# Optimization experiments

Measured on AMD Instinct MI355X. Metric: run time of the kernel, lower is better.

The kernel has to match this reference:

```python
import jax, jax.numpy as jnp
import numpy as np

N = 32768      # number of nodes (joint candidates)
DIN = 128      # NODE_INPUT_DIM
H1 = 128       # OUTPUT_SIZES[0]
DOUT = 128     # OUTPUT_SIZES[-1] == output_dim
T = 17         # number of node types / expert MLPs


def setup_inputs() -> dict:
    key = jax.random.key(0)
    ks = jax.random.split(key, 6)
    x = jax.random.normal(ks[0], (N, DIN), dtype=jnp.float32)
    node_types = jax.random.randint(ks[1], (N,), 0, T)
    # Stacked per-type MLP parameters (17 independent Linear-ReLU-Linear MLPs).
    W1 = jax.random.normal(ks[2], (T, DIN, H1), dtype=jnp.float32) / np.float32(np.sqrt(DIN))
    b1 = jax.random.normal(ks[3], (T, H1), dtype=jnp.float32) * 0.01
    W2 = jax.random.normal(ks[4], (T, H1, DOUT), dtype=jnp.float32) / np.float32(np.sqrt(H1))
    b2 = jax.random.normal(ks[5], (T, DOUT), dtype=jnp.float32) * 0.01
    return {"x": x, "W1": W1, "b1": b1, "W2": W2, "b2": b2, "node_types": node_types}


def reference(x, W1, b1, W2, b2, node_types):
    # Dense hard-routing: evaluate all 17 type-specific MLPs on every node,
    # then select each node's own type. Mathematically identical to the
    # boolean-mask gather/scatter loop in the torch module (each row of the
    # output is MLP_{node_types[n]}(x[n])), but fully vectorized and jittable.
    h = jax.nn.relu(jnp.einsum('nd,tdh->nth', x, W1) + b1)   # [N, T, H1]
    y = jnp.einsum('nth,thm->ntm', h, W2) + b2               # [N, T, DOUT]
    # gather the row matching each node's type (combine step)
    out = jnp.take_along_axis(y, node_types[:, None, None], axis=1)[:, 0, :]  # [N, DOUT]
    return out
```

## Files before the change

### kernel.cpp

```cpp
#include <hip/hip_runtime.h>

#define N_NODES 32768
#define NB 128
#define DIM 128
#define NT 17
#define ROWS 64
#define BPT 48
#define LP 136

typedef short bf16x8 __attribute__((ext_vector_type(8)));
typedef float f32x4 __attribute__((ext_vector_type(4)));

#define WS_BLOCKHIST 0
#define WS_TL        8704
#define WS_W1T       74240
#define WS_W2T       631296

__device__ __forceinline__ unsigned short f2bf(float f) {
  unsigned int u = __float_as_uint(f);
  u += 0x7FFFu + ((u >> 16) & 1u);
  return (unsigned short)(u >> 16);
}

__global__ void k_pre(const int* __restrict__ types, int* __restrict__ blockHist,
                      unsigned short* __restrict__ tl,
                      const float* __restrict__ W1, const float* __restrict__ W2,
                      unsigned short* __restrict__ W1t, unsigned short* __restrict__ W2t) {
  int tid = threadIdx.x;
  if (blockIdx.x < NB) {
    __shared__ int h[NT];
    if (tid < NT) h[tid] = 0;
    __syncthreads();
    int i = blockIdx.x * 256 + tid;
    int ty = types[i];
    int r = atomicAdd(&h[ty], 1);
    tl[i] = (unsigned short)(ty | (r << 5));
    __syncthreads();
    if (tid < NT) blockHist[blockIdx.x * NT + tid] = h[tid];
    return;
  }
  int m = blockIdx.x - NB;
  const float* src = (m < NT) ? (W1 + (size_t)m * DIM * DIM)
                              : (W2 + (size_t)(m - NT) * DIM * DIM);
  unsigned short* dst = (m < NT) ? (W1t + (size_t)m * DIM * DIM)
                                 : (W2t + (size_t)(m - NT) * DIM * DIM);
  __shared__ unsigned short tile[DIM * LP];
  #pragma unroll
  for (int it = 0; it < 32; ++it) {
    int s = tid + it * 256;
    int n = s & 127, kp = s >> 7;
    float a = src[(size_t)(2 * kp) * DIM + n];
    float b = src[(size_t)(2 * kp + 1) * DIM + n];
    unsigned int pk = (unsigned int)f2bf(a) | ((unsigned int)f2bf(b) << 16);
    *(unsigned int*)&tile[n * LP + 2 * kp] = pk;
  }
  __syncthreads();
  #pragma unroll
  for (int it = 0; it < 8; ++it) {
    int s = tid + it * 256;
    int n = s >> 4, c = s & 15;
    *(uint4*)(dst + (size_t)n * DIM + c * 8) = *(const uint4*)&tile[n * LP + c * 8];
  }
}

__global__ __launch_bounds__(256, 3)
void k_mlp(const float* __restrict__ x, const float* __restrict__ b1,
           const float* __restrict__ b2, float* __restrict__ out,
           const int* __restrict__ blockHist, const unsigned short* __restrict__ tl,
           const unsigned short* __restrict__ W1t, const unsigned short* __restrict__ W2t) {
  int t = blockIdx.y;
  int tid = threadIdx.x;

  __shared__ int cc[NB];
  __shared__ int prow[ROWS];
  __shared__ unsigned short Xs[ROWS * LP];
  __shared__ unsigned short Ws[DIM * LP];

  int v = 0;
  if (tid < NB) { v = blockHist[tid * NT + t]; cc[tid] = v; }
  #pragma unroll
  for (int off = 1; off < NB; off <<= 1) {
    __syncthreads();
    int add = (tid < NB && tid >= off) ? cc[tid - off] : 0;
    __syncthreads();
    if (tid < NB) { v += add; cc[tid] = v; }
  }
  __syncthreads();
  int total = cc[NB - 1];
  int win_lo = blockIdx.x * ROWS;
  if (win_lo >= total) return;
  int win_hi = win_lo + ROWS;
  int nvalid = min(ROWS, total - win_lo);

  if (tid < ROWS) prow[tid] = 0;
  __syncthreads();

  int lo = 0, hi = NB;
  while (lo < hi) { int mid = (lo + hi) >> 1; if (cc[mid] > win_lo) hi = mid; else lo = mid + 1; }
  for (int b = lo; b < NB; ++b) {
    int excl = b ? cc[b - 1] : 0;
    if (excl >= win_hi) break;
    unsigned short pv = tl[b * 256 + tid];
    int ty = pv & 31, lr = pv >> 5;
    int g = excl + lr;
    if (ty == t && g >= win_lo && g < win_hi) prow[g - win_lo] = b * 256 + tid;
  }
  __syncthreads();

  #pragma unroll
  for (int it = 0; it < 8; ++it) {
    int s = tid + it * 256;
    int r = s >> 5, c4 = s & 31;
    int rr = (r < nvalid) ? r : 0;
    const float4 vx = *(const float4*)(x + (size_t)prow[rr] * DIM + c4 * 4);
    unsigned int lo2 = (unsigned int)f2bf(vx.x) | ((unsigned int)f2bf(vx.y) << 16);
    unsigned int hi2 = (unsigned int)f2bf(vx.z) | ((unsigned int)f2bf(vx.w) << 16);
    *(uint2*)&Xs[r * LP + c4 * 4] = make_uint2(lo2, hi2);
  }
  const unsigned short* w1g = W1t + (size_t)t * DIM * DIM;
  #pragma unroll
  for (int it = 0; it < 8; ++it) {
    int s = tid + it * 256;
    int n = s >> 4, c = s & 15;
    *(uint4*)&Ws[n * LP + c * 8] = *(const uint4*)(w1g + n * DIM + c * 8);
  }
  __syncthreads();

  int lane = tid & 63, w = tid >> 6;
  int l15 = lane & 15, q = lane >> 4;
  int arow = w * 16 + l15;
  int kb = q * 8;

  f32x4 acc[8];
  #pragma unroll
  for (int nt = 0; nt < 8; ++nt) acc[nt] = (f32x4){0.f, 0.f, 0.f, 0.f};
  #pragma unroll
  for (int kk = 0; kk < 4; ++kk) {
    bf16x8 a = *(const bf16x8*)&Xs[arow * LP + kk * 32 + kb];
    #pragma unroll
    for (int nt = 0; nt < 8; ++nt) {
      bf16x8 b = *(const bf16x8*)&Ws[(nt * 16 + l15) * LP + kk * 32 + kb];
      acc[nt] = __builtin_amdgcn_mfma_f32_16x16x32_bf16(a, b, acc[nt], 0, 0, 0);
    }
  }
  const float* b1t = b1 + t * DIM;
  #pragma unroll
  for (int nt = 0; nt < 8; ++nt) {
    int col = nt * 16 + l15;
    float bias = b1t[col];
    #pragma unroll
    for (int r = 0; r < 4; ++r) {
      int row = w * 16 + q * 4 + r;
      Xs[row * LP + col] = f2bf(fmaxf(acc[nt][r] + bias, 0.f));
    }
  }
  __syncthreads();

  const unsigned short* w2g = W2t + (size_t)t * DIM * DIM;
  #pragma unroll
  for (int it = 0; it < 8; ++it) {
    int s = tid + it * 256;
    int n = s >> 4, c = s & 15;
    *(uint4*)&Ws[n * LP + c * 8] = *(const uint4*)(w2g + n * DIM + c * 8);
  }
  __syncthreads();

  #pragma unroll
  for (int nt = 0; nt < 8; ++nt) acc[nt] = (f32x4){0.f, 0.f, 0.f, 0.f};
  #pragma unroll
  for (int kk = 0; kk < 4; ++kk) {
    bf16x8 a = *(const bf16x8*)&Xs[arow * LP + kk * 32 + kb];
    #pragma unroll
    for (int nt = 0; nt < 8; ++nt) {
      bf16x8 b = *(const bf16x8*)&Ws[(nt * 16 + l15) * LP + kk * 32 + kb];
      acc[nt] = __builtin_amdgcn_mfma_f32_16x16x32_bf16(a, b, acc[nt], 0, 0, 0);
    }
  }
  const float* b2t = b2 + t * DIM;
  int r0 = w * 16 + q * 4;
  int gr[4]; bool vld[4];
  #pragma unroll
  for (int r = 0; r < 4; ++r) {
    vld[r] = (r0 + r) < nvalid;
    gr[r] = prow[r0 + r];
  }
  #pragma unroll
  for (int nt = 0; nt < 8; ++nt) {
    int col = nt * 16 + l15;
    float bias = b2t[col];
    #pragma unroll
    for (int r = 0; r < 4; ++r) {
      if (vld[r]) out[(size_t)gr[r] * DIM + col] = acc[nt][r] + bias;
    }
  }
}

extern "C" void kernel_launch(void* const* d_in, const int* in_sizes, int n_in,
                              void* d_out, int out_size, void* d_ws, size_t ws_size,
                              hipStream_t stream) {
  const float* x  = (const float*)d_in[0];
  const float* W1 = (const float*)d_in[1];
  const float* b1 = (const float*)d_in[2];
  const float* W2 = (const float*)d_in[3];
  const float* b2 = (const float*)d_in[4];
  const int* types = (const int*)d_in[5];
  float* out = (float*)d_out;

  char* ws = (char*)d_ws;
  int* blockHist = (int*)(ws + WS_BLOCKHIST);
  unsigned short* tl  = (unsigned short*)(ws + WS_TL);
  unsigned short* W1t = (unsigned short*)(ws + WS_W1T);
  unsigned short* W2t = (unsigned short*)(ws + WS_W2T);

  k_pre<<<NB + 2 * NT, 256, 0, stream>>>(types, blockHist, tl, W1, W2, W1t, W2t);
  dim3 grid(BPT, NT);
  k_mlp<<<grid, 256, 0, stream>>>(x, b1, b2, out, blockHist, tl, W1t, W2t);
}
```

Baseline: 94.65 us.

## Double rows per block to 128 and prefetch type-list loads in gather loop

Each block now handles 128 rows of a node type instead of 64, with each wave computing two 16-row MFMA tiles that share each loaded weight fragment. This halves the number of blocks that each reload the per-type W1/W2 tiles into LDS and the per-block scan/search overhead. The row-gather loop now software-prefetches the next type-list chunk, and the zeroing of the prow array before it is removed. Occupancy hint drops from 3 to 2 blocks per CU, and the larger tile means fewer blocks and more padding waste on partially filled windows.

```diff
diff --git a/kernel.cpp b/kernel.cpp
--- a/kernel.cpp
+++ b/kernel.cpp
@@ -4,8 +4,8 @@
 #define NB 128
 #define DIM 128
 #define NT 17
-#define ROWS 64
-#define BPT 48
+#define ROWS 128
+#define BPT 24
 #define LP 136
 
 typedef short bf16x8 __attribute__((ext_vector_type(8)));
@@ -63,7 +63,7 @@
   }
 }
 
-__global__ __launch_bounds__(256, 3)
+__global__ __launch_bounds__(256, 2)
 void k_mlp(const float* __restrict__ x, const float* __restrict__ b1,
            const float* __restrict__ b2, float* __restrict__ out,
            const int* __restrict__ blockHist, const unsigned short* __restrict__ tl,
@@ -92,23 +92,27 @@
   int win_hi = win_lo + ROWS;
   int nvalid = min(ROWS, total - win_lo);
 
-  if (tid < ROWS) prow[tid] = 0;
-  __syncthreads();
-
-  int lo = 0, hi = NB;
-  while (lo < hi) { int mid = (lo + hi) >> 1; if (cc[mid] > win_lo) hi = mid; else lo = mid + 1; }
-  for (int b = lo; b < NB; ++b) {
-    int excl = b ? cc[b - 1] : 0;
-    if (excl >= win_hi) break;
+  {
+    int lo = 0, hi = NB;
+    while (lo < hi) { int mid = (lo + hi) >> 1; if (cc[mid] > win_lo) hi = mid; else lo = mid + 1; }
+    int b = lo;
     unsigned short pv = tl[b * 256 + tid];
-    int ty = pv & 31, lr = pv >> 5;
-    int g = excl + lr;
-    if (ty == t && g >= win_lo && g < win_hi) prow[g - win_lo] = b * 256 + tid;
-  }
-  __syncthreads();
-
-  #pragma unroll
-  for (int it = 0; it < 8; ++it) {
+    while (true) {
+      int excl = b ? cc[b - 1] : 0;
+      bool last = (b + 1 >= NB) || (cc[b] >= win_hi);
+      unsigned short nv = 0;
+      if (!last) nv = tl[(b + 1) * 256 + tid];
+      int ty = pv & 31, lr = pv >> 5;
+      int g = excl + lr;
+      if (ty == t && g >= win_lo && g < win_hi) prow[g - win_lo] = b * 256 + tid;
+      if (last) break;
+      pv = nv; ++b;
+    }
+  }
+  __syncthreads();
+
+  #pragma unroll
+  for (int it = 0; it < 16; ++it) {
     int s = tid + it * 256;
     int r = s >> 5, c4 = s & 31;
     int rr = (r < nvalid) ? r : 0;
@@ -128,19 +132,23 @@
 
   int lane = tid & 63, w = tid >> 6;
   int l15 = lane & 15, q = lane >> 4;
-  int arow = w * 16 + l15;
   int kb = q * 8;
-
-  f32x4 acc[8];
-  #pragma unroll
-  for (int nt = 0; nt < 8; ++nt) acc[nt] = (f32x4){0.f, 0.f, 0.f, 0.f};
+  int arow0 = w * 32 + l15;
+
+  f32x4 acc[2][8];
+  #pragma unroll
+  for (int mt = 0; mt < 2; ++mt)
+    #pragma unroll
+    for (int nt = 0; nt < 8; ++nt) acc[mt][nt] = (f32x4){0.f, 0.f, 0.f, 0.f};
   #pragma unroll
   for (int kk = 0; kk < 4; ++kk) {
-    bf16x8 a = *(const bf16x8*)&Xs[arow * LP + kk * 32 + kb];
+    bf16x8 a0 = *(const bf16x8*)&Xs[arow0 * LP + kk * 32 + kb];
+    bf16x8 a1 = *(const bf16x8*)&Xs[(arow0 + 16) * LP + kk * 32 + kb];
     #pragma unroll
     for (int nt = 0; nt < 8; ++nt) {
       bf16x8 b = *(const bf16x8*)&Ws[(nt * 16 + l15) * LP + kk * 32 + kb];
-      acc[nt] = __builtin_amdgcn_mfma_f32_16x16x32_bf16(a, b, acc[nt], 0, 0, 0);
+      acc[0][nt] = __builtin_amdgcn_mfma_f32_16x16x32_bf16(a0, b, acc[0][nt], 0, 0, 0);
+      acc[1][nt] = __builtin_amdgcn_mfma_f32_16x16x32_bf16(a1, b, acc[1][nt], 0, 0, 0);
     }
   }
   const float* b1t = b1 + t * DIM;
@@ -149,10 +157,12 @@
     int col = nt * 16 + l15;
     float bias = b1t[col];
     #pragma unroll
-    for (int r = 0; r < 4; ++r) {
-      int row = w * 16 + q * 4 + r;
-      Xs[row * LP + col] = f2bf(fmaxf(acc[nt][r] + bias, 0.f));
-    }
+    for (int mt = 0; mt < 2; ++mt)
+      #pragma unroll
+      for (int r = 0; r < 4; ++r) {
+        int row = w * 32 + mt * 16 + q * 4 + r;
+        Xs[row * LP + col] = f2bf(fmaxf(acc[mt][nt][r] + bias, 0.f));
+      }
   }
   __syncthreads();
 
@@ -166,32 +176,32 @@
   __syncthreads();
 
   #pragma unroll
-  for (int nt = 0; nt < 8; ++nt) acc[nt] = (f32x4){0.f, 0.f, 0.f, 0.f};
+  for (int mt = 0; mt < 2; ++mt)
+    #pragma unroll
+    for (int nt = 0; nt < 8; ++nt) acc[mt][nt] = (f32x4){0.f, 0.f, 0.f, 0.f};
   #pragma unroll
   for (int kk = 0; kk < 4; ++kk) {
-    bf16x8 a = *(const bf16x8*)&Xs[arow * LP + kk * 32 + kb];
+    bf16x8 a0 = *(const bf16x8*)&Xs[arow0 * LP + kk * 32 + kb];
+    bf16x8 a1 = *(const bf16x8*)&Xs[(arow0 + 16) * LP + kk * 32 + kb];
     #pragma unroll
     for (int nt = 0; nt < 8; ++nt) {
       bf16x8 b = *(const bf16x8*)&Ws[(nt * 16 + l15) * LP + kk * 32 + kb];
-      acc[nt] = __builtin_amdgcn_mfma_f32_16x16x32_bf16(a, b, acc[nt], 0, 0, 0);
+      acc[0][nt] = __builtin_amdgcn_mfma_f32_16x16x32_bf16(a0, b, acc[0][nt], 0, 0, 0);
+      acc[1][nt] = __builtin_amdgcn_mfma_f32_16x16x32_bf16(a1, b, acc[1][nt], 0, 0, 0);
     }
   }
   const float* b2t = b2 + t * DIM;
-  int r0 = w * 16 + q * 4;
-  int gr[4]; bool vld[4];
-  #pragma unroll
-  for (int r = 0; r < 4; ++r) {
-    vld[r] = (r0 + r) < nvalid;
-    gr[r] = prow[r0 + r];
-  }
   #pragma unroll
   for (int nt = 0; nt < 8; ++nt) {
     int col = nt * 16 + l15;
     float bias = b2t[col];
     #pragma unroll
-    for (int r = 0; r < 4; ++r) {
-      if (vld[r]) out[(size_t)gr[r] * DIM + col] = acc[nt][r] + bias;
-    }
+    for (int mt = 0; mt < 2; ++mt)
+      #pragma unroll
+      for (int r = 0; r < 4; ++r) {
+        int lr = w * 32 + mt * 16 + q * 4 + r;
+        if (lr < nvalid) out[(size_t)prow[lr] * DIM + col] = acc[mt][nt][r] + bias;
+      }
   }
 }
 
```

Result: slower. 99.08 us (+4.7%).
